# Performance work log

Measured on AMD Instinct MI355X. Metric: run time of the kernel, lower is better.

Reference implementation:

```python
import jax, jax.numpy as jnp
import numpy as np

N = 30000      # num nodes (cells)
E = 480000     # num edges (avg degree 16)
D_IN = 1000    # input_dim (genes)
H = 8          # nheads
F_H = 32       # hidden_dim per head
D_EMB = 64     # embedding_dim
NEG_SLOPE = 0.2


def setup_inputs() -> dict:
    key = jax.random.key(0)
    ks = jax.random.split(key, 12)
    glorot = lambda k, shape, fan: (jax.random.normal(k, shape, jnp.float32)
                                    * (1.0 / np.sqrt(fan)))
    return {
        "x": jax.random.normal(ks[0], (N, D_IN), jnp.float32),
        "edge_index": jax.random.randint(ks[1], (2, E), 0, N),
        "edge_weight": jax.random.uniform(ks[2], (E,), jnp.float32),
        # GATConv params
        "W": glorot(ks[3], (D_IN, H * F_H), D_IN),
        "att_src": glorot(ks[4], (H, F_H), F_H),
        "att_dst": glorot(ks[5], (H, F_H), F_H),
        "bias_gat": jnp.zeros((H * F_H,), jnp.float32),
        # embedding Linear
        "emb_W": glorot(ks[6], (H * F_H, D_EMB), H * F_H),
        "emb_b": jnp.zeros((D_EMB,), jnp.float32),
        # decoder MLP
        "dec_W1": glorot(ks[7], (D_EMB, F_H), D_EMB),
        "dec_b1": jnp.zeros((F_H,), jnp.float32),
        "dec_W2": glorot(ks[8], (F_H, D_IN), F_H),
        "dec_b2": jnp.zeros((D_IN,), jnp.float32),
    }


def _gat_conv(x, edge_index, W, att_src, att_dst, bias):
    n = x.shape[0]
    h = (x @ W).reshape(n, H, F_H)                    # [N,H,F]
    a_s = jnp.einsum('nhf,hf->nh', h, att_src)        # [N,H]
    a_d = jnp.einsum('nhf,hf->nh', h, att_dst)        # [N,H]
    # add self loops (PyG default add_self_loops=True)
    loops = jnp.arange(n)
    src = jnp.concatenate([edge_index[0], loops])     # [E+N]
    dst = jnp.concatenate([edge_index[1], loops])     # [E+N]
    logits = jax.nn.leaky_relu(a_s[src] + a_d[dst], NEG_SLOPE)  # [E+N,H]
    # segment softmax over incoming edges of each destination node
    m = jax.ops.segment_max(logits, dst, num_segments=n)        # [N,H]
    p = jnp.exp(logits - m[dst])
    denom = jax.ops.segment_sum(p, dst, num_segments=n)         # [N,H]
    alpha = p / denom[dst]                                      # [E+N,H]
    msg = h[src] * alpha[:, :, None]                            # [E+N,H,F]
    out = jax.ops.segment_sum(msg, dst, num_segments=n)         # [N,H,F]
    return out.reshape(n, H * F_H) + bias


def reference(x, edge_index, edge_weight, W, att_src, att_dst, bias_gat,
              emb_W, emb_b, dec_W1, dec_b1, dec_W2, dec_b2):
    # edge_weight is accepted but unused: PyG GATConv with edge_dim=None has
    # no edge-feature pathway.
    h = jax.nn.relu(_gat_conv(x, edge_index, W, att_src, att_dst, bias_gat))
    z = h @ emb_W + emb_b                               # [N, D_EMB]
    d = jax.nn.relu(z @ dec_W1 + dec_b1)                # [N, F_H]
    recon = d @ dec_W2 + dec_b2                         # [N, D_IN]
    return recon, z
```

## Files before the change

kernel.cpp:

```cpp
#include <hip/hip_runtime.h>
#include <hip/hip_bf16.h>

#define N_NODES 30000
#define N_EDGES 480000
#define D_IN    1000
#define KPAD    1024
#define NHEAD   8
#define F_HID   32
#define D_EMB   64
#define NEG_SLOPE 0.2f
#define MAXDEG  64

typedef __attribute__((ext_vector_type(4))) float  f32x4;
typedef __attribute__((ext_vector_type(8))) __bf16 bf16x8;
typedef __attribute__((ext_vector_type(4))) __bf16 bf16x4;

#define WT_TOT    (256*KPAD + D_EMB*256 + F_HID*D_EMB + D_IN*F_HID)
#define WT_BLOCKS ((WT_TOT + 255) / 256)
#define WA_BLOCKS (16 * KPAD / 256)
#define ZC_BLOCKS ((N_NODES + 255) / 256)

__global__ __launch_bounds__(256) void cvt_w(
    const float* __restrict__ W, const float* __restrict__ emb_W,
    const float* __restrict__ d1, const float* __restrict__ d2,
    const float* __restrict__ att_src, const float* __restrict__ att_dst,
    __bf16* __restrict__ WbT, __bf16* __restrict__ embT,
    __bf16* __restrict__ d1T, __bf16* __restrict__ d2T,
    __bf16* __restrict__ WaT, int* __restrict__ cnt)
{
    int b = blockIdx.x;
    if (b < WT_BLOCKS) {
        int i = b * 256 + threadIdx.x;
        if (i < 256 * KPAD) {
            int n = i >> 10, k = i & 1023;
            WbT[i] = (k < D_IN) ? (__bf16)W[(size_t)k * 256 + n] : (__bf16)0.0f;
            return;
        }
        i -= 256 * KPAD;
        if (i < D_EMB * 256) {
            int n = i >> 8, k = i & 255;
            embT[i] = (__bf16)emb_W[(size_t)k * D_EMB + n];
            return;
        }
        i -= D_EMB * 256;
        if (i < F_HID * D_EMB) {
            int n = i >> 6, k = i & 63;
            d1T[i] = (__bf16)d1[(size_t)k * F_HID + n];
            return;
        }
        i -= F_HID * D_EMB;
        if (i < D_IN * F_HID) {
            int n = i >> 5, k = i & 31;
            d2T[i] = (__bf16)d2[(size_t)k * D_IN + n];
        }
        return;
    }
    b -= WT_BLOCKS;
    if (b < WA_BLOCKS) {
        int i = b * 256 + threadIdx.x;
        int j = i >> 10, k = i & 1023;
        float s = 0.f;
        if (k < D_IN) {
            const float* av = (j < 8 ? att_src : att_dst) + (j & 7) * F_HID;
            const float* wr = W + (size_t)k * 256 + (j & 7) * F_HID;
            #pragma unroll
            for (int f = 0; f < F_HID; f++) s += wr[f] * av[f];
        }
        WaT[i] = (__bf16)s;
        return;
    }
    b -= WA_BLOCKS;
    {
        int i = b * 256 + threadIdx.x;
        if (i < N_NODES) cnt[i] = 0;
    }
}

#define SC_BLOCKS  ((N_EDGES + 255) / 256)

__global__ __launch_bounds__(256) void edge_scatter(
    const int* __restrict__ eidx, int* __restrict__ cnt, int* __restrict__ slots)
{
    int e = blockIdx.x * 256 + threadIdx.x;
    if (e < N_EDGES) {
        int d = eidx[N_EDGES + e];
        int slot = atomicAdd(&cnt[d], 1);
        slots[d * MAXDEG + slot] = eidx[e];
    }
}

__device__ __forceinline__ void stage_tile(
    __bf16* lds, const __bf16* __restrict__ g, int base, int maxr,
    int K, int k0, int rows, int w, int lane, int stride)
{
    const int rsub = lane >> 2;
    const int c    = lane & 3;
    for (int off = w * 1024; off < rows * 64; off += stride) {
        int r  = (off >> 6) + rsub;
        int gr = base + r; gr = gr > maxr ? maxr : gr;
        int chunk = c ^ (r & 3);
        const __bf16* gp = g + (size_t)gr * K + k0 + chunk * 8;
        __builtin_amdgcn_global_load_lds(
            (const __attribute__((address_space(1))) void*)gp,
            (__attribute__((address_space(3))) void*)((char*)lds + off),
            16, 0, 0);
    }
}

template<int BM, int BN, int RELU>
__global__ __launch_bounds__(256) void gemm_bf16(
    const __bf16* __restrict__ A, const __bf16* __restrict__ Bt,
    float* __restrict__ Cf, __bf16* __restrict__ Cb,
    const float* __restrict__ bias, int M, int Nn, int K)
{
    constexpr int MT = BM / 32;
    constexpr int NT = BN / 32;
    __shared__ __align__(16) __bf16 As[BM * 32];
    __shared__ __align__(16) __bf16 Bs[BN * 32];

    const int tid  = threadIdx.x;
    const int w    = tid >> 6, lane = tid & 63;
    const int wm   = w >> 1,   wn   = w & 1;
    const int quad = lane >> 4, l16 = lane & 15;
    const int bm = blockIdx.x * BM, bn = blockIdx.y * BN;

    f32x4 acc[MT][NT];
    #pragma unroll
    for (int i = 0; i < MT; i++)
        #pragma unroll
        for (int j = 0; j < NT; j++)
            acc[i][j] = (f32x4){0.f, 0.f, 0.f, 0.f};

    for (int k0 = 0; k0 < K; k0 += 32) {
        stage_tile(As, A,  bm, M  - 1, K, k0, BM, w, lane, 4096);
        stage_tile(Bs, Bt, bn, Nn - 1, K, k0, BN, w, lane, 4096);
        __syncthreads();

        bf16x8 af[MT], bfr[NT];
        #pragma unroll
        for (int mt = 0; mt < MT; mt++) {
            int r = wm * 64 + mt * 16 + l16;
            af[mt] = *(const bf16x8*)&As[r * 32 + (quad ^ (r & 3)) * 8];
        }
        #pragma unroll
        for (int nt = 0; nt < NT; nt++) {
            int r = wn * (NT * 16) + nt * 16 + l16;
            bfr[nt] = *(const bf16x8*)&Bs[r * 32 + (quad ^ (r & 3)) * 8];
        }
        #pragma unroll
        for (int mt = 0; mt < MT; mt++)
            #pragma unroll
            for (int nt = 0; nt < NT; nt++)
                acc[mt][nt] = __builtin_amdgcn_mfma_f32_16x16x32_bf16(
                    af[mt], bfr[nt], acc[mt][nt], 0, 0, 0);
        __syncthreads();
    }

    #pragma unroll
    for (int nt = 0; nt < NT; nt++) {
        int col = bn + wn * (NT * 16) + nt * 16 + l16;
        if (col >= Nn) continue;
        float bv = bias ? bias[col] : 0.0f;
        #pragma unroll
        for (int mt = 0; mt < MT; mt++) {
            int row0 = bm + wm * 64 + mt * 16 + quad * 4;
            #pragma unroll
            for (int rr = 0; rr < 4; rr++) {
                int row = row0 + rr;
                if (row < M) {
                    float v = acc[mt][nt][rr] + bv;
                    if (RELU) v = v > 0.f ? v : 0.f;
                    if (Cf) Cf[(size_t)row * Nn + col] = v;
                    if (Cb) Cb[(size_t)row * Nn + col] = (__bf16)v;
                }
            }
        }
    }
}

__device__ __forceinline__ void xload8(const float* __restrict__ xrow, int cb,
                                       f32x4& u0, f32x4& u1)
{
    if (cb < D_IN) {
        const f32x4* p = (const f32x4*)(xrow + cb);
        u0 = p[0]; u1 = p[1];
    } else {
        u0 = (f32x4){0.f, 0.f, 0.f, 0.f};
        u1 = (f32x4){0.f, 0.f, 0.f, 0.f};
    }
}

__device__ __forceinline__ bf16x8 cvt8(const f32x4& u0, const f32x4& u1)
{
    bf16x8 o;
    o[0] = (__bf16)u0.x; o[1] = (__bf16)u0.y; o[2] = (__bf16)u0.z; o[3] = (__bf16)u0.w;
    o[4] = (__bf16)u1.x; o[5] = (__bf16)u1.y; o[6] = (__bf16)u1.z; o[7] = (__bf16)u1.w;
    return o;
}

__global__ __launch_bounds__(512, 2) void gemm1_fused(
    const float* __restrict__ x, const __bf16* __restrict__ WbT,
    const __bf16* __restrict__ WaT, __bf16* __restrict__ hb,
    float* __restrict__ a_s, float* __restrict__ a_d, int M)
{
    __shared__ __align__(16) __bf16 As[2][128 * 32];
    __shared__ __align__(16) __bf16 Bs[2][256 * 32];

    const int tid  = threadIdx.x;
    const int w    = tid >> 6, lane = tid & 63;
    const int wm   = w >> 2,   wn   = w & 3;
    const int quad = lane >> 4, l16 = lane & 15;
    const int bm   = blockIdx.x * 128;

    const int r0   = tid >> 2;
    const int cpos = tid & 3;
    const int cxor = (cpos ^ (r0 & 3)) << 3;
    int grow = bm + r0; if (grow > M - 1) grow = M - 1;
    const float* xrow = x + (size_t)grow * D_IN;

    const int brsub = lane >> 2;
    const int bc    = lane & 3;

    f32x4 acc[4][4];
    #pragma unroll
    for (int i = 0; i < 4; i++)
        #pragma unroll
        for (int j = 0; j < 4; j++)
            acc[i][j] = (f32x4){0.f, 0.f, 0.f, 0.f};
    f32x4 accA[4];
    #pragma unroll
    for (int i = 0; i < 4; i++) accA[i] = (f32x4){0.f, 0.f, 0.f, 0.f};

    const bool att = (wn == 0);
    const __bf16* warow = WaT + (size_t)l16 * KPAD + quad * 8;

    auto stageB = [&](int buf, int k0) {
        #pragma unroll
        for (int off = 0; off < 16384; off += 8192) {
            int o2 = off + w * 1024;
            int r = (o2 >> 6) + brsub;
            int chunk = bc ^ (r & 3);
            const __bf16* gp = WbT + (size_t)r * KPAD + k0 + chunk * 8;
            __builtin_amdgcn_global_load_lds(
                (const __attribute__((address_space(1))) void*)gp,
                (__attribute__((address_space(3))) void*)((char*)&Bs[buf][0] + o2),
                16, 0, 0);
        }
    };

    auto compute = [&](int buf, const bf16x8& attfrag) {
        bf16x8 af[4], bfr[4];
        #pragma unroll
        for (int mt = 0; mt < 4; mt++) {
            int r = wm * 64 + mt * 16 + l16;
            af[mt] = *(const bf16x8*)&As[buf][r * 32 + (quad ^ (r & 3)) * 8];
        }
        #pragma unroll
        for (int nt = 0; nt < 4; nt++) {
            int r = wn * 64 + nt * 16 + l16;
            bfr[nt] = *(const bf16x8*)&Bs[buf][r * 32 + (quad ^ (r & 3)) * 8];
        }
        #pragma unroll
        for (int mt = 0; mt < 4; mt++)
            #pragma unroll
            for (int nt = 0; nt < 4; nt++)
                acc[mt][nt] = __builtin_amdgcn_mfma_f32_16x16x32_bf16(
                    af[mt], bfr[nt], acc[mt][nt], 0, 0, 0);
        if (att) {
            #pragma unroll
            for (int mt = 0; mt < 4; mt++)
                accA[mt] = __builtin_amdgcn_mfma_f32_16x16x32_bf16(
                    af[mt], attfrag, accA[mt], 0, 0, 0);
        }
    };

    f32x4 xa0, xa1, xb0, xb1;
    bf16x8 attEv = {}, attOd = {};

    xload8(xrow, 0 + cxor, xa0, xa1);
    xload8(xrow, 32 + cxor, xb0, xb1);
    if (att) attEv = *(const bf16x8*)(warow + 0);
    *(bf16x8*)&As[0][r0 * 32 + cpos * 8] = cvt8(xa0, xa1);
    stageB(0, 0);
    __syncthreads();

    for (int k0 = 0; k0 < KPAD; k0 += 64) {
        xload8(xrow, (k0 + 64) + cxor, xa0, xa1);
        if (att) attOd = *(const bf16x8*)(warow + k0 + 32);
        *(bf16x8*)&As[1][r0 * 32 + cpos * 8] = cvt8(xb0, xb1);
        stageB(1, k0 + 32);
        compute(0, attEv);
        __syncthreads();

        if (k0 + 64 < KPAD) {
            xload8(xrow, (k0 + 96) + cxor, xb0, xb1);
            if (att) attEv = *(const bf16x8*)(warow + k0 + 64);
            *(bf16x8*)&As[0][r0 * 32 + cpos * 8] = cvt8(xa0, xa1);
            stageB(0, k0 + 64);
        }
        compute(1, attOd);
        __syncthreads();
    }

    #pragma unroll
    for (int nt = 0; nt < 4; nt++) {
        int col = wn * 64 + nt * 16 + l16;
        #pragma unroll
        for (int mt = 0; mt < 4; mt++) {
            int row0 = bm + wm * 64 + mt * 16 + quad * 4;
            #pragma unroll
            for (int rr = 0; rr < 4; rr++) {
                int row = row0 + rr;
                if (row < M)
                    hb[(size_t)row * 256 + col] = (__bf16)acc[mt][nt][rr];
            }
        }
    }
    if (att) {
        #pragma unroll
        for (int mt = 0; mt < 4; mt++) {
            int row0 = bm + wm * 64 + mt * 16 + quad * 4;
            #pragma unroll
            for (int rr = 0; rr < 4; rr++) {
                int row = row0 + rr;
                if (row < M) {
                    float v = accA[mt][rr];
                    if (l16 < 8) a_s[row * NHEAD + l16] = v;
                    else         a_d[row * NHEAD + (l16 - 8)] = v;
                }
            }
        }
    }
}

__device__ __forceinline__ float leaky(float x) {
    return x > 0.f ? x : NEG_SLOPE * x;
}

__global__ __launch_bounds__(256) void gat_aggregate(
    const __bf16* __restrict__ hb, const float* __restrict__ a_s,
    const float* __restrict__ a_d, const int* __restrict__ cnt,
    const int* __restrict__ slots, const float* __restrict__ bias,
    __bf16* __restrict__ hgatb)
{
    const int wid  = threadIdx.x >> 6;
    const int lane = threadIdx.x & 63;
    const int n = blockIdx.x * 4 + wid;
    if (n >= N_NODES) return;

    const int hh = lane >> 3;
    const int fo = (lane & 7) * 4;
    const int base = n * MAXDEG;
    const int c = cnt[n];
    const float adn = a_d[n * NHEAD + hh];

    float p = __expf(leaky(a_s[n * NHEAD + hh] + adn));
    float denom = p;
    f32x4 acc;
    {
        bf16x4 hv = *(const bf16x4*)(hb + (size_t)n * 256 + hh * F_HID + fo);
        acc.x = p * (float)hv[0]; acc.y = p * (float)hv[1];
        acc.z = p * (float)hv[2]; acc.w = p * (float)hv[3];
    }
    int e = 0;
    for (; e + 4 <= c; e += 4) {
        const int4 ss = *(const int4*)(slots + base + e);
        int s0 = ss.x, s1 = ss.y, s2 = ss.z, s3 = ss.w;
        float l0 = a_s[s0 * NHEAD + hh], l1 = a_s[s1 * NHEAD + hh];
        float l2 = a_s[s2 * NHEAD + hh], l3 = a_s[s3 * NHEAD + hh];
        bf16x4 h0 = *(const bf16x4*)(hb + (size_t)s0 * 256 + hh * F_HID + fo);
        bf16x4 h1 = *(const bf16x4*)(hb + (size_t)s1 * 256 + hh * F_HID + fo);
        bf16x4 h2 = *(const bf16x4*)(hb + (size_t)s2 * 256 + hh * F_HID + fo);
        bf16x4 h3 = *(const bf16x4*)(hb + (size_t)s3 * 256 + hh * F_HID + fo);
        float p0 = __expf(leaky(l0 + adn)), p1 = __expf(leaky(l1 + adn));
        float p2 = __expf(leaky(l2 + adn)), p3 = __expf(leaky(l3 + adn));
        denom += (p0 + p1) + (p2 + p3);
        acc.x += p0*(float)h0[0] + p1*(float)h1[0] + p2*(float)h2[0] + p3*(float)h3[0];
        acc.y += p0*(float)h0[1] + p1*(float)h1[1] + p2*(float)h2[1] + p3*(float)h3[1];
        acc.z += p0*(float)h0[2] + p1*(float)h1[2] + p2*(float)h2[2] + p3*(float)h3[2];
        acc.w += p0*(float)h0[3] + p1*(float)h1[3] + p2*(float)h2[3] + p3*(float)h3[3];
    }
    for (; e < c; e++) {
        int s = slots[base + e];
        float pe = __expf(leaky(a_s[s * NHEAD + hh] + adn));
        denom += pe;
        bf16x4 hv = *(const bf16x4*)(hb + (size_t)s * 256 + hh * F_HID + fo);
        acc.x += pe * (float)hv[0]; acc.y += pe * (float)hv[1];
        acc.z += pe * (float)hv[2]; acc.w += pe * (float)hv[3];
    }
    float inv = 1.0f / denom;
    f32x4 bv = *(const f32x4*)(bias + lane * 4);
    float o0 = acc.x * inv + bv.x, o1 = acc.y * inv + bv.y;
    float o2 = acc.z * inv + bv.z, o3 = acc.w * inv + bv.w;
    o0 = o0 > 0.f ? o0 : 0.f;
    o1 = o1 > 0.f ? o1 : 0.f;
    o2 = o2 > 0.f ? o2 : 0.f;
    o3 = o3 > 0.f ? o3 : 0.f;
    bf16x4 ob;
    ob[0] = (__bf16)o0; ob[1] = (__bf16)o1; ob[2] = (__bf16)o2; ob[3] = (__bf16)o3;
    *(bf16x4*)(hgatb + (size_t)n * 256 + lane * 4) = ob;
}

__global__ __launch_bounds__(256) void gemm_zd(
    const __bf16* __restrict__ hgatb, const __bf16* __restrict__ embT,
    const __bf16* __restrict__ d1T, const float* __restrict__ emb_b,
    const float* __restrict__ dec_b1, float* __restrict__ z,
    __bf16* __restrict__ dbufb, int M)
{
    __shared__ __align__(16) __bf16 As[128 * 32];
    __shared__ __align__(16) __bf16 Bs[64 * 32];
    __shared__ __align__(16) __bf16 zS[128 * 64];
    __shared__ __align__(16) __bf16 Bs2[2 * 32 * 32];

    const int tid  = threadIdx.x;
    const int w    = tid >> 6, lane = tid & 63;
    const int wm   = w >> 1,   wn   = w & 1;
    const int quad = lane >> 4, l16 = lane & 15;
    const int bm = blockIdx.x * 128;

    stage_tile(Bs2,        d1T, 0, 31, 64, 0,  32, w, lane, 4096);
    stage_tile(Bs2 + 1024, d1T, 0, 31, 64, 32, 32, w, lane, 4096);

    f32x4 acc[4][2];
    #pragma unroll
    for (int i = 0; i < 4; i++) { acc[i][0] = (f32x4){0,0,0,0}; acc[i][1] = (f32x4){0,0,0,0}; }

    for (int k0 = 0; k0 < 256; k0 += 32) {
        stage_tile(As, hgatb, bm, M - 1, 256, k0, 128, w, lane, 4096);
        stage_tile(Bs, embT,  0,  D_EMB - 1, 256, k0, 64, w, lane, 4096);
        __syncthreads();
        bf16x8 af[4], bfr[2];
        #pragma unroll
        for (int mt = 0; mt < 4; mt++) {
            int r = wm * 64 + mt * 16 + l16;
            af[mt] = *(const bf16x8*)&As[r * 32 + (quad ^ (r & 3)) * 8];
        }
        #pragma unroll
        for (int nt = 0; nt < 2; nt++) {
            int r = wn * 32 + nt * 16 + l16;
            bfr[nt] = *(const bf16x8*)&Bs[r * 32 + (quad ^ (r & 3)) * 8];
        }
        #pragma unroll
        for (int mt = 0; mt < 4; mt++)
            #pragma unroll
            for (int nt = 0; nt < 2; nt++)
                acc[mt][nt] = __builtin_amdgcn_mfma_f32_16x16x32_bf16(
                    af[mt], bfr[nt], acc[mt][nt], 0, 0, 0);
        __syncthreads();
    }

    #pragma unroll
    for (int nt = 0; nt < 2; nt++) {
        int col = wn * 32 + nt * 16 + l16;
        float bv = emb_b[col];
        int t = col >> 5, cch = (col >> 3) & 3, j = col & 7;
        #pragma unroll
        for (int mt = 0; mt < 4; mt++) {
            int rl0 = wm * 64 + mt * 16 + quad * 4;
            #pragma unroll
            for (int rr = 0; rr < 4; rr++) {
                int rl = rl0 + rr;
                int row = bm + rl;
                float v = acc[mt][nt][rr] + bv;
                if (row < M) z[(size_t)row * D_EMB + col] = v;
                zS[t * 4096 + rl * 32 + (cch ^ (rl & 3)) * 8 + j] = (__bf16)v;
            }
        }
    }
    __syncthreads();

    f32x4 accd[4];
    #pragma unroll
    for (int i = 0; i < 4; i++) accd[i] = (f32x4){0,0,0,0};
    #pragma unroll
    for (int t = 0; t < 2; t++) {
        bf16x8 af[4], bfr;
        #pragma unroll
        for (int mt = 0; mt < 4; mt++) {
            int r = wm * 64 + mt * 16 + l16;
            af[mt] = *(const bf16x8*)&zS[t * 4096 + r * 32 + (quad ^ (r & 3)) * 8];
        }
        {
            int r = wn * 16 + l16;
            bfr = *(const bf16x8*)&Bs2[t * 1024 + r * 32 + (quad ^ (r & 3)) * 8];
        }
        #pragma unroll
        for (int mt = 0; mt < 4; mt++)
            accd[mt] = __builtin_amdgcn_mfma_f32_16x16x32_bf16(af[mt], bfr, accd[mt], 0, 0, 0);
    }
    {
        int col = wn * 16 + l16;
        float bv = dec_b1[col];
        #pragma unroll
        for (int mt = 0; mt < 4; mt++) {
            int rl0 = wm * 64 + mt * 16 + quad * 4;
            #pragma unroll
            for (int rr = 0; rr < 4; rr++) {
                int row = bm + rl0 + rr;
                if (row < M) {
                    float v = accd[mt][rr] + bv;
                    v = v > 0.f ? v : 0.f;
                    dbufb[(size_t)row * F_HID + col] = (__bf16)v;
                }
            }
        }
    }
}

extern "C" void kernel_launch(void* const* d_in, const int* in_sizes, int n_in,
                              void* d_out, int out_size, void* d_ws, size_t ws_size,
                              hipStream_t stream)
{
    const float* x        = (const float*)d_in[0];
    const int*   eidx     = (const int*)  d_in[1];
    const float* W        = (const float*)d_in[3];
    const float* att_src  = (const float*)d_in[4];
    const float* att_dst  = (const float*)d_in[5];
    const float* bias_gat = (const float*)d_in[6];
    const float* emb_W    = (const float*)d_in[7];
    const float* emb_b    = (const float*)d_in[8];
    const float* dec_W1   = (const float*)d_in[9];
    const float* dec_b1   = (const float*)d_in[10];
    const float* dec_W2   = (const float*)d_in[11];
    const float* dec_b2   = (const float*)d_in[12];

    float* out   = (float*)d_out;
    float* recon = out;
    float* z     = out + (size_t)N_NODES * D_IN;

    char* ws = (char*)d_ws;
    size_t o = 0;
    auto alloc = [&](size_t bytes) { char* p = ws + o; o = (o + bytes + 255) & ~(size_t)255; return p; };
    __bf16* hb      = (__bf16*)alloc((size_t)N_NODES * 256 * 2);
    __bf16* WbT     = (__bf16*)alloc((size_t)256 * KPAD * 2);
    __bf16* embT    = (__bf16*)alloc((size_t)D_EMB * 256 * 2);
    __bf16* d1T     = (__bf16*)alloc((size_t)F_HID * D_EMB * 2);
    __bf16* d2T     = (__bf16*)alloc((size_t)D_IN * F_HID * 2);
    __bf16* WaT     = (__bf16*)alloc((size_t)16 * KPAD * 2);
    __bf16* hgatb   = (__bf16*)alloc((size_t)N_NODES * 256 * 2);
    __bf16* dbufb   = (__bf16*)alloc((size_t)N_NODES * F_HID * 2);
    float*  a_s     = (float*) alloc((size_t)N_NODES * NHEAD * 4);
    float*  a_d     = (float*) alloc((size_t)N_NODES * NHEAD * 4);
    int*    slots   = (int*)   alloc((size_t)N_NODES * MAXDEG * 4);
    int*    cnt     = (int*)   alloc((size_t)N_NODES * 4);

    const int MB = (N_NODES + 127) / 128;

    cvt_w<<<WT_BLOCKS + WA_BLOCKS + ZC_BLOCKS, 256, 0, stream>>>(
        W, emb_W, dec_W1, dec_W2, att_src, att_dst,
        WbT, embT, d1T, d2T, WaT, cnt);

    edge_scatter<<<SC_BLOCKS, 256, 0, stream>>>(eidx, cnt, slots);

    gemm1_fused<<<MB, 512, 0, stream>>>(x, WbT, WaT, hb, a_s, a_d, N_NODES);

    gat_aggregate<<<N_NODES / 4, 256, 0, stream>>>(
        hb, a_s, a_d, cnt, slots, bias_gat, hgatb);

    gemm_zd<<<MB, 256, 0, stream>>>(
        hgatb, embT, d1T, emb_b, dec_b1, z, dbufb, N_NODES);

    gemm_bf16<128, 128, 0><<<dim3(MB, 8), 256, 0, stream>>>(
        dbufb, d2T, recon, (__bf16*)nullptr, dec_b2, N_NODES, D_IN, F_HID);
}
```

Baseline: 409.1 us.

## Fuse decoder output GEMM into z/d kernel and edge scatter into GEMM1

```diff
diff --git a/kernel.cpp b/kernel.cpp
--- a/kernel.cpp
+++ b/kernel.cpp
@@ -73,19 +73,6 @@
     {
         int i = b * 256 + threadIdx.x;
         if (i < N_NODES) cnt[i] = 0;
-    }
-}
-
-#define SC_BLOCKS  ((N_EDGES + 255) / 256)
-
-__global__ __launch_bounds__(256) void edge_scatter(
-    const int* __restrict__ eidx, int* __restrict__ cnt, int* __restrict__ slots)
-{
-    int e = blockIdx.x * 256 + threadIdx.x;
-    if (e < N_EDGES) {
-        int d = eidx[N_EDGES + e];
-        int slot = atomicAdd(&cnt[d], 1);
-        slots[d * MAXDEG + slot] = eidx[e];
     }
 }
 
@@ -107,76 +94,8 @@
     }
 }
 
-template<int BM, int BN, int RELU>
-__global__ __launch_bounds__(256) void gemm_bf16(
-    const __bf16* __restrict__ A, const __bf16* __restrict__ Bt,
-    float* __restrict__ Cf, __bf16* __restrict__ Cb,
-    const float* __restrict__ bias, int M, int Nn, int K)
-{
-    constexpr int MT = BM / 32;
-    constexpr int NT = BN / 32;
-    __shared__ __align__(16) __bf16 As[BM * 32];
-    __shared__ __align__(16) __bf16 Bs[BN * 32];
-
-    const int tid  = threadIdx.x;
-    const int w    = tid >> 6, lane = tid & 63;
-    const int wm   = w >> 1,   wn   = w & 1;
-    const int quad = lane >> 4, l16 = lane & 15;
-    const int bm = blockIdx.x * BM, bn = blockIdx.y * BN;
-
-    f32x4 acc[MT][NT];
-    #pragma unroll
-    for (int i = 0; i < MT; i++)
-        #pragma unroll
-        for (int j = 0; j < NT; j++)
-            acc[i][j] = (f32x4){0.f, 0.f, 0.f, 0.f};
-
-    for (int k0 = 0; k0 < K; k0 += 32) {
-        stage_tile(As, A,  bm, M  - 1, K, k0, BM, w, lane, 4096);
-        stage_tile(Bs, Bt, bn, Nn - 1, K, k0, BN, w, lane, 4096);
-        __syncthreads();
-
-        bf16x8 af[MT], bfr[NT];
-        #pragma unroll
-        for (int mt = 0; mt < MT; mt++) {
-            int r = wm * 64 + mt * 16 + l16;
-            af[mt] = *(const bf16x8*)&As[r * 32 + (quad ^ (r & 3)) * 8];
-        }
-        #pragma unroll
-        for (int nt = 0; nt < NT; nt++) {
-            int r = wn * (NT * 16) + nt * 16 + l16;
-            bfr[nt] = *(const bf16x8*)&Bs[r * 32 + (quad ^ (r & 3)) * 8];
-        }
-        #pragma unroll
-        for (int mt = 0; mt < MT; mt++)
-            #pragma unroll
-            for (int nt = 0; nt < NT; nt++)
-                acc[mt][nt] = __builtin_amdgcn_mfma_f32_16x16x32_bf16(
-                    af[mt], bfr[nt], acc[mt][nt], 0, 0, 0);
-        __syncthreads();
-    }
-
-    #pragma unroll
-    for (int nt = 0; nt < NT; nt++) {
-        int col = bn + wn * (NT * 16) + nt * 16 + l16;
-        if (col >= Nn) continue;
-        float bv = bias ? bias[col] : 0.0f;
-        #pragma unroll
-        for (int mt = 0; mt < MT; mt++) {
-            int row0 = bm + wm * 64 + mt * 16 + quad * 4;
-            #pragma unroll
-            for (int rr = 0; rr < 4; rr++) {
-                int row = row0 + rr;
-                if (row < M) {
-                    float v = acc[mt][nt][rr] + bv;
-                    if (RELU) v = v > 0.f ? v : 0.f;
-                    if (Cf) Cf[(size_t)row * Nn + col] = v;
-                    if (Cb) Cb[(size_t)row * Nn + col] = (__bf16)v;
-                }
-            }
-        }
-    }
-}
+#define GEMM1_BLOCKS ((N_NODES + 127) / 128)
+#define SC512        ((N_EDGES + 511) / 512)
 
 __device__ __forceinline__ void xload8(const float* __restrict__ xrow, int cb,
                                        f32x4& u0, f32x4& u1)
@@ -201,10 +120,22 @@
 __global__ __launch_bounds__(512, 2) void gemm1_fused(
     const float* __restrict__ x, const __bf16* __restrict__ WbT,
     const __bf16* __restrict__ WaT, __bf16* __restrict__ hb,
-    float* __restrict__ a_s, float* __restrict__ a_d, int M)
+    float* __restrict__ a_s, float* __restrict__ a_d,
+    const int* __restrict__ eidx, int* __restrict__ cnt,
+    int* __restrict__ slots, int M)
 {
     __shared__ __align__(16) __bf16 As[2][128 * 32];
     __shared__ __align__(16) __bf16 Bs[2][256 * 32];
+
+    if (blockIdx.x >= GEMM1_BLOCKS) {
+        int e = (blockIdx.x - GEMM1_BLOCKS) * 512 + threadIdx.x;
+        if (e < N_EDGES) {
+            int d = eidx[N_EDGES + e];
+            int slot = atomicAdd(&cnt[d], 1);
+            slots[d * MAXDEG + slot] = eidx[e];
+        }
+        return;
+    }
 
     const int tid  = threadIdx.x;
     const int w    = tid >> 6, lane = tid & 63;
@@ -401,16 +332,19 @@
     *(bf16x4*)(hgatb + (size_t)n * 256 + lane * 4) = ob;
 }
 
-__global__ __launch_bounds__(256) void gemm_zd(
+__global__ __launch_bounds__(256) void gemm_zdr(
     const __bf16* __restrict__ hgatb, const __bf16* __restrict__ embT,
-    const __bf16* __restrict__ d1T, const float* __restrict__ emb_b,
-    const float* __restrict__ dec_b1, float* __restrict__ z,
-    __bf16* __restrict__ dbufb, int M)
-{
-    __shared__ __align__(16) __bf16 As[128 * 32];
-    __shared__ __align__(16) __bf16 Bs[64 * 32];
-    __shared__ __align__(16) __bf16 zS[128 * 64];
-    __shared__ __align__(16) __bf16 Bs2[2 * 32 * 32];
+    const __bf16* __restrict__ d1T, const __bf16* __restrict__ d2T,
+    const float* __restrict__ emb_b, const float* __restrict__ dec_b1,
+    const float* __restrict__ dec_b2, float* __restrict__ z,
+    float* __restrict__ recon, int M)
+{
+    __shared__ __align__(16) __bf16 smem[49152];
+    __bf16* As  = smem;
+    __bf16* Bs  = smem + 4096;
+    __bf16* zS  = smem + 6144;
+    __bf16* Bs2 = smem + 14336;
+    __bf16* d2S = smem + 16384;
 
     const int tid  = threadIdx.x;
     const int w    = tid >> 6, lane = tid & 63;
@@ -428,6 +362,10 @@
     for (int k0 = 0; k0 < 256; k0 += 32) {
         stage_tile(As, hgatb, bm, M - 1, 256, k0, 128, w, lane, 4096);
         stage_tile(Bs, embT,  0,  D_EMB - 1, 256, k0, 64, w, lane, 4096);
+        {
+            int t = k0 >> 5;
+            stage_tile(d2S + t * 4096, d2T, t * 128, D_IN - 1, 32, 0, 128, w, lane, 4096);
+        }
         __syncthreads();
         bf16x8 af[4], bfr[2];
         #pragma unroll
@@ -491,16 +429,46 @@
     {
         int col = wn * 16 + l16;
         float bv = dec_b1[col];
+        int cc = col >> 3, j = col & 7;
         #pragma unroll
         for (int mt = 0; mt < 4; mt++) {
             int rl0 = wm * 64 + mt * 16 + quad * 4;
             #pragma unroll
             for (int rr = 0; rr < 4; rr++) {
-                int row = bm + rl0 + rr;
-                if (row < M) {
-                    float v = accd[mt][rr] + bv;
-                    v = v > 0.f ? v : 0.f;
-                    dbufb[(size_t)row * F_HID + col] = (__bf16)v;
+                int rl = rl0 + rr;
+                float v = accd[mt][rr] + bv;
+                v = v > 0.f ? v : 0.f;
+                As[rl * 32 + (cc ^ (rl & 3)) * 8 + j] = (__bf16)v;
+            }
+        }
+    }
+    __syncthreads();
+
+    bf16x8 daf[4];
+    #pragma unroll
+    for (int mt = 0; mt < 4; mt++) {
+        int r = wm * 64 + mt * 16 + l16;
+        daf[mt] = *(const bf16x8*)&As[r * 32 + (quad ^ (r & 3)) * 8];
+    }
+    for (int tt = wn; tt < 63; tt += 2) {
+        int col = tt * 16 + l16;
+        bf16x8 bfr = *(const bf16x8*)&d2S[(size_t)col * 32 + (quad ^ (col & 3)) * 8];
+        f32x4 a[4];
+        #pragma unroll
+        for (int mt = 0; mt < 4; mt++) {
+            a[mt] = (f32x4){0.f, 0.f, 0.f, 0.f};
+            a[mt] = __builtin_amdgcn_mfma_f32_16x16x32_bf16(daf[mt], bfr, a[mt], 0, 0, 0);
+        }
+        if (col < D_IN) {
+            float bv = dec_b2[col];
+            #pragma unroll
+            for (int mt = 0; mt < 4; mt++) {
+                int row0 = bm + wm * 64 + mt * 16 + quad * 4;
+                #pragma unroll
+                for (int rr = 0; rr < 4; rr++) {
+                    int row = row0 + rr;
+                    if (row < M)
+                        recon[(size_t)row * D_IN + col] = a[mt][rr] + bv;
                 }
             }
         }
@@ -538,28 +506,21 @@
     __bf16* d2T     = (__bf16*)alloc((size_t)D_IN * F_HID * 2);
     __bf16* WaT     = (__bf16*)alloc((size_t)16 * KPAD * 2);
     __bf16* hgatb   = (__bf16*)alloc((size_t)N_NODES * 256 * 2);
-    __bf16* dbufb   = (__bf16*)alloc((size_t)N_NODES * F_HID * 2);
     float*  a_s     = (float*) alloc((size_t)N_NODES * NHEAD * 4);
     float*  a_d     = (float*) alloc((size_t)N_NODES * NHEAD * 4);
     int*    slots   = (int*)   alloc((size_t)N_NODES * MAXDEG * 4);
     int*    cnt     = (int*)   alloc((size_t)N_NODES * 4);
 
-    const int MB = (N_NODES + 127) / 128;
-
     cvt_w<<<WT_BLOCKS + WA_BLOCKS + ZC_BLOCKS, 256, 0, stream>>>(
         W, emb_W, dec_W1, dec_W2, att_src, att_dst,
         WbT, embT, d1T, d2T, WaT, cnt);
 
-    edge_scatter<<<SC_BLOCKS, 256, 0, stream>>>(eidx, cnt, slots);
-
-    gemm1_fused<<<MB, 512, 0, stream>>>(x, WbT, WaT, hb, a_s, a_d, N_NODES);
+    gemm1_fused<<<GEMM1_BLOCKS + SC512, 512, 0, stream>>>(
+        x, WbT, WaT, hb, a_s, a_d, eidx, cnt, slots, N_NODES);
 
     gat_aggregate<<<N_NODES / 4, 256, 0, stream>>>(
         hb, a_s, a_d, cnt, slots, bias_gat, hgatb);
 
-    gemm_zd<<<MB, 256, 0, stream>>>(
-        hgatb, embT, d1T, emb_b, dec_b1, z, dbufb, N_NODES);
-
-    gemm_bf16<128, 128, 0><<<dim3(MB, 8), 256, 0, stream>>>(
-        dbufb, d2T, recon, (__bf16*)nullptr, dec_b2, N_NODES, D_IN, F_HID);
-}
+    gemm_zdr<<<GEMM1_BLOCKS, 256, 0, stream>>>(
+        hgatb, embT, d1T, d2T, emb_b, dec_b1, dec_b2, z, recon, N_NODES);
+}
```

After: 397.6 us. -2.8%, faster.
